# Kernel optimization log

Hardware: AMD Instinct MI355X
Metric: run time of the kernel (lower is better)

The kernel has to match this reference:

```python
import jax, jax.numpy as jnp
import numpy as np

HEADS = 8
NQ = 4  # n_qubits


def _apply_rx(state, q, theta):
    # state: (M,2,2,2,2) complex, theta: (M,)
    c = jnp.cos(theta / 2).astype(jnp.complex64)
    s = (-1j * jnp.sin(theta / 2)).astype(jnp.complex64)
    g = jnp.stack([jnp.stack([c, s], -1), jnp.stack([s, c], -1)], -2)  # (M,2,2)
    st = jnp.moveaxis(state, 1 + q, 1)
    st = jnp.einsum('mab,mb...->ma...', g, st)
    return jnp.moveaxis(st, 1, 1 + q)


def _apply_cnot(state, c, t):
    st = jnp.moveaxis(state, [1 + c, 1 + t], [1, 2])  # (M,2(ctrl),2(tgt),...)
    st = jnp.concatenate([st[:, :1], st[:, 1:, ::-1]], axis=1)
    return jnp.moveaxis(st, [1, 2], [1 + c, 1 + t])


def vqc(x, weights):
    # x: (M,4) embedding angles; weights: (L,4) layer RX angles
    M = x.shape[0]
    state = jnp.zeros((M, 2, 2, 2, 2), jnp.complex64).at[:, 0, 0, 0, 0].set(1.0)
    for q in range(NQ):  # AngleEmbedding (RX)
        state = _apply_rx(state, q, x[:, q])
    for l in range(weights.shape[0]):  # BasicEntanglerLayers
        for q in range(NQ):
            state = _apply_rx(state, q, jnp.broadcast_to(weights[l, q], (M,)))
        for q in range(NQ):
            state = _apply_cnot(state, q, (q + 1) % NQ)
    probs = state.real ** 2 + state.imag ** 2  # (M,2,2,2,2)
    z = [jnp.moveaxis(probs, 1 + q, 1)[:, 0].sum((1, 2, 3))
         - jnp.moveaxis(probs, 1 + q, 1)[:, 1].sum((1, 2, 3)) for q in range(NQ)]
    return jnp.stack(z, -1)  # (M,4) PauliZ expvals


def setup_inputs() -> dict:
    key = jax.random.key(0)
    ks = jax.random.split(key, 24)
    B, S, E = 16, 512, 512
    D = E // HEADS
    f = jax.random.normal
    inp = {
        'query': f(ks[0], (B, S, E), jnp.float32),
        'key': f(ks[1], (B, S, E), jnp.float32),
        'value': f(ks[2], (B, S, E), jnp.float32),
        'mask': jnp.ones((B, S, S), jnp.int32),
        'Wq_in': f(ks[3], (NQ, D), jnp.float32) / np.sqrt(D),
        'bq_in': f(ks[4], (NQ,), jnp.float32) / np.sqrt(D),
        'Wk_in': f(ks[5], (NQ, D), jnp.float32) / np.sqrt(D),
        'bk_in': f(ks[6], (NQ,), jnp.float32) / np.sqrt(D),
        'Wv_in': f(ks[7], (NQ, D), jnp.float32) / np.sqrt(D),
        'bv_in': f(ks[8], (NQ,), jnp.float32) / np.sqrt(D),
        'wvq': f(ks[9], (1, NQ), jnp.float32),
        'wvk': f(ks[10], (1, NQ), jnp.float32),
        'wvv': f(ks[11], (1, NQ), jnp.float32),
        'Wq': f(ks[12], (D, NQ), jnp.float32) / np.sqrt(NQ),
        'bq': f(ks[13], (D,), jnp.float32) / np.sqrt(NQ),
        'Wk': f(ks[14], (D, NQ), jnp.float32) / np.sqrt(NQ),
        'bk': f(ks[15], (D,), jnp.float32) / np.sqrt(NQ),
        'Wv': f(ks[16], (D, NQ), jnp.float32) / np.sqrt(NQ),
        'bv': f(ks[17], (D,), jnp.float32) / np.sqrt(NQ),
        'Wo': f(ks[18], (E, 2 * E), jnp.float32) / np.sqrt(2 * E),
        'bo': f(ks[19], (E,), jnp.float32) / np.sqrt(2 * E),
    }
    return inp


def reference(query, key, value, mask, Wq_in, bq_in, Wk_in, bk_in, Wv_in, bv_in,
              wvq, wvk, wvv, Wq, bq, Wk, bk, Wv, bv, Wo, bo):
    B, S, E = query.shape
    H = HEADS
    D = E // H

    def project(x, W_in, b_in, w_vqc, W_out, b_out):
        xh = x.reshape(B, S, H, D)
        xin = jnp.einsum('bshd,qd->bshq', xh, W_in) + b_in  # (B,S,H,NQ)
        xq = vqc(xin.reshape(-1, NQ), w_vqc).reshape(B, S, H, NQ)
        return jnp.einsum('bshq,dq->bshd', xq, W_out) + b_out  # (B,S,H,D)

    Q = project(query, Wq_in, bq_in, wvq, Wq, bq)
    K = project(key, Wk_in, bk_in, wvk, Wk, bk)
    V = project(value, Wv_in, bv_in, wvv, Wv, bv)

    energy = jnp.einsum('bqhd,bkhd->bhqk', Q, K)
    # NOTE: original masked_fill result is discarded (no-op); scale is depth/2
    # due to Python precedence (depth**1/2 == depth/2). Reproduced faithfully.
    attn = jax.nn.softmax(energy / (D / 2.0), axis=-1)
    out = jnp.einsum('bhqv,bvhd->bqhd', attn, V).reshape(B, S, H * D)
    Qf = Q.reshape(B, S, H * D)
    cat = jnp.concatenate([Qf, out], axis=-1)  # (B,S,2E)
    return cat @ Wo.T + bo
```

## Files before the change

kernel.cpp:

```cpp
#include <hip/hip_runtime.h>
#include <hip/hip_bf16.h>

#define B_ 16
#define S_ 512
#define E_ 512
#define H_ 8
#define D_ 64

typedef __hip_bfloat16 bf16;
typedef unsigned short u16;
typedef __attribute__((ext_vector_type(8))) short short8;
typedef __attribute__((ext_vector_type(4))) float floatx4;

__device__ __forceinline__ u16 f2b(float x) {
    bf16 h = __float2bfloat16(x);
    return *reinterpret_cast<u16*>(&h);
}
__device__ __forceinline__ short8 ld8(const u16* p) { return *(const short8*)p; }

__global__ __launch_bounds__(256) void wconv_kernel(
    const float* __restrict__ Wo, u16* __restrict__ Wb)
{
    const int i = (blockIdx.x * 256 + threadIdx.x) * 8;
    const float4 a = *(const float4*)&Wo[i];
    const float4 b = *(const float4*)&Wo[i + 4];
    u16 tmp[8] __attribute__((aligned(16)));
    tmp[0] = f2b(a.x); tmp[1] = f2b(a.y); tmp[2] = f2b(a.z); tmp[3] = f2b(a.w);
    tmp[4] = f2b(b.x); tmp[5] = f2b(b.y); tmp[6] = f2b(b.z); tmp[7] = f2b(b.w);
    *(short8*)&Wb[i] = *(short8*)tmp;
}

__global__ __launch_bounds__(256) void proj_kernel(
    const float* __restrict__ q_in, const float* __restrict__ k_in, const float* __restrict__ v_in,
    const float* __restrict__ Wq_in, const float* __restrict__ bq_in,
    const float* __restrict__ Wk_in, const float* __restrict__ bk_in,
    const float* __restrict__ Wv_in, const float* __restrict__ bv_in,
    const float* __restrict__ wvq, const float* __restrict__ wvk, const float* __restrict__ wvv,
    const float* __restrict__ Wq, const float* __restrict__ bq,
    const float* __restrict__ Wk, const float* __restrict__ bk,
    const float* __restrict__ Wv, const float* __restrict__ bv,
    u16* __restrict__ Qb, u16* __restrict__ Kb, u16* __restrict__ Vb)
{
    const int wave = threadIdx.x >> 6;
    const int lane = threadIdx.x & 63;
    const int g = blockIdx.x * 4 + wave;
    const int p = g >> 16;
    const int m = g & 0xFFFF;
    const int h = m & 7;
    const int s = (m >> 3) & 511;
    const int b = m >> 12;

    const float *X, *Win, *bin, *wv, *Wout, *bout;
    u16* dst;
    if (p == 0)      { X = q_in; Win = Wq_in; bin = bq_in; wv = wvq; Wout = Wq; bout = bq; dst = Qb; }
    else if (p == 1) { X = k_in; Win = Wk_in; bin = bk_in; wv = wvk; Wout = Wk; bout = bk; dst = Kb; }
    else             { X = v_in; Win = Wv_in; bin = bv_in; wv = wvv; Wout = Wv; bout = bv; dst = Vb; }

    const int q = lane >> 4;
    const int dsub = lane & 15;
    const float* xp = X + ((size_t)(b * S_ + s)) * E_ + h * 64;
    const float* wp = Win + q * 64;

    float part = 0.f;
#pragma unroll
    for (int j = 0; j < 4; ++j)
        part += xp[dsub + 16 * j] * wp[dsub + 16 * j];
#pragma unroll
    for (int off = 8; off >= 1; off >>= 1)
        part += __shfl_xor(part, off, 64);

    const float theta = part + bin[q] + wv[q];
    const float c  = __cosf(theta);
    const float ca = __shfl_xor(c, 16, 64);
    const float cb = __shfl_xor(c, 32, 64);
    const float cd = __shfl_xor(ca, 32, 64);

    const float c0 = (q == 0) ? c : (q == 1) ? ca : (q == 2) ? cb : cd;
    const float c1 = (q == 1) ? c : (q == 0) ? ca : (q == 3) ? cb : cd;
    const float c2 = (q == 2) ? c : (q == 3) ? ca : (q == 0) ? cb : cd;
    const float c3 = (q == 3) ? c : (q == 2) ? ca : (q == 1) ? cb : cd;

    const float z0 = c1 * c2 * c3;
    const float z1 = c0 * c1;
    const float z2 = z1 * c2;
    const float z3 = z2 * c3;

    const float4 wo = *(const float4*)&Wout[lane * 4];
    const float out = z0 * wo.x + z1 * wo.y + z2 * wo.z + z3 * wo.w + bout[lane];
    dst[(((size_t)(b * H_ + h)) * S_ + s) * D_ + lane] = f2b(out);
}

__global__ __launch_bounds__(256) void attn_kernel(
    const u16* __restrict__ Qb, const u16* __restrict__ Kb, const u16* __restrict__ Vb,
    u16* __restrict__ Ob)
{
    __shared__ __align__(16) u16 Ks[64][72];
    __shared__ __align__(16) u16 Vt[64][72];
    __shared__ __align__(16) u16 Ps[4][16][80];

    const int t = threadIdx.x, lane = t & 63, w = t >> 6;
    const int bh = blockIdx.x >> 3;
    const int q0 = (blockIdx.x & 7) * 64;
    const int b = bh >> 3, h = bh & 7;

    const u16* Qp = Qb + (size_t)bh * (S_ * D_) + (size_t)q0 * D_;
    const u16* Kp = Kb + (size_t)bh * (S_ * D_);
    const u16* Vp = Vb + (size_t)bh * (S_ * D_);

    const int nl = lane & 15;
    const int kg = (lane >> 4) * 8;

    const short8 qa0 = ld8(&Qp[(w * 16 + nl) * 64 + kg]);
    const short8 qa1 = ld8(&Qp[(w * 16 + nl) * 64 + kg + 32]);

    floatx4 of[4];
    float l_run[4] = {0.f, 0.f, 0.f, 0.f};
#pragma unroll
    for (int nt = 0; nt < 4; ++nt) of[nt] = 0.f;

    for (int ch = 0; ch < 8; ++ch) {
        __syncthreads();
        for (int i = t; i < 512; i += 256) {
            const int r = i & 63, c = (i >> 6) * 8;
            *(short8*)&Ks[r][c] = ld8(&Kp[(ch * 64 + r) * 64 + c]);
        }
        for (int i = t; i < 512; i += 256) {
            const int r = i & 63, c = (i >> 6) * 8;
            short8 v = ld8(&Vp[(ch * 64 + r) * 64 + c]);
#pragma unroll
            for (int j = 0; j < 8; ++j) Vt[c + j][r] = (u16)((short*)&v)[j];
        }
        __syncthreads();

        floatx4 sf[4];
#pragma unroll
        for (int nt = 0; nt < 4; ++nt) sf[nt] = 0.f;
#pragma unroll
        for (int nt = 0; nt < 4; ++nt) {
            sf[nt] = __builtin_amdgcn_mfma_f32_16x16x32_bf16(qa0, ld8(&Ks[nt * 16 + nl][kg]), sf[nt], 0, 0, 0);
            sf[nt] = __builtin_amdgcn_mfma_f32_16x16x32_bf16(qa1, ld8(&Ks[nt * 16 + nl][kg + 32]), sf[nt], 0, 0, 0);
        }

        const int prow = (lane >> 4) * 4;
#pragma unroll
        for (int nt = 0; nt < 4; ++nt) {
#pragma unroll
            for (int r = 0; r < 4; ++r) {
                const float pv = __expf(sf[nt][r] * 0.03125f);
                l_run[r] += pv;
                Ps[w][prow + r][nt * 16 + nl] = f2b(pv);
            }
        }

        const short8 pa0 = ld8(&Ps[w][nl][kg]);
        const short8 pa1 = ld8(&Ps[w][nl][kg + 32]);
#pragma unroll
        for (int nt = 0; nt < 4; ++nt) {
            of[nt] = __builtin_amdgcn_mfma_f32_16x16x32_bf16(pa0, ld8(&Vt[nt * 16 + nl][kg]), of[nt], 0, 0, 0);
            of[nt] = __builtin_amdgcn_mfma_f32_16x16x32_bf16(pa1, ld8(&Vt[nt * 16 + nl][kg + 32]), of[nt], 0, 0, 0);
        }
    }

    float inv[4];
#pragma unroll
    for (int r = 0; r < 4; ++r) {
        float sum = l_run[r];
#pragma unroll
        for (int off = 1; off < 16; off <<= 1) sum += __shfl_xor(sum, off, 64);
        inv[r] = 1.0f / sum;
    }
    const int srow = q0 + w * 16 + (lane >> 4) * 4;
#pragma unroll
    for (int r = 0; r < 4; ++r) {
        const size_t base = ((size_t)(b * S_ + srow + r)) * E_ + h * 64 + nl;
#pragma unroll
        for (int nt = 0; nt < 4; ++nt)
            Ob[base + nt * 16] = f2b(of[nt][r] * inv[r]);
    }
}

__global__ __launch_bounds__(256) void out_kernel(
    const u16* __restrict__ Qb, const u16* __restrict__ Ob,
    const u16* __restrict__ Wb, const float* __restrict__ bo,
    float* __restrict__ out)
{
    __shared__ __align__(16) u16 As[64][72];
    __shared__ __align__(16) u16 Bs[128][72];

    const int t = threadIdx.x, lane = t & 63, w = t >> 6;
    const int e0 = (blockIdx.x & 3) * 128;
    const int n0 = (blockIdx.x >> 2) * 64;
    const int wr = (w >> 1) * 32, wc = (w & 1) * 64;
    const int nl = lane & 15, kg = (lane >> 4) * 8;

    floatx4 acc[2][4];
#pragma unroll
    for (int i = 0; i < 2; ++i)
#pragma unroll
        for (int j = 0; j < 4; ++j) acc[i][j] = 0.f;

    for (int j0 = 0; j0 < 1024; j0 += 64) {
        for (int i = t; i < 512; i += 256) {
            const int r = i & 63, c = (i >> 6) * 8;
            const int n = n0 + r;
            const u16* src = (j0 < 512)
                ? &Qb[(((size_t)(n >> 9) * 8 + (j0 >> 6)) * 512 + (n & 511)) * 64 + c]
                : &Ob[(size_t)n * 512 + (j0 - 512) + c];
            *(short8*)&As[r][c] = ld8(src);
        }
        for (int i = t; i < 1024; i += 256) {
            const int r = i & 127, c = (i >> 7) * 8;
            *(short8*)&Bs[r][c] = ld8(&Wb[(size_t)(e0 + r) * 1024 + j0 + c]);
        }
        __syncthreads();

        short8 af[2][2], bfr[4][2];
#pragma unroll
        for (int mt = 0; mt < 2; ++mt) {
            af[mt][0] = ld8(&As[wr + mt * 16 + nl][kg]);
            af[mt][1] = ld8(&As[wr + mt * 16 + nl][kg + 32]);
        }
#pragma unroll
        for (int nt = 0; nt < 4; ++nt) {
            bfr[nt][0] = ld8(&Bs[wc + nt * 16 + nl][kg]);
            bfr[nt][1] = ld8(&Bs[wc + nt * 16 + nl][kg + 32]);
        }
#pragma unroll
        for (int mt = 0; mt < 2; ++mt)
#pragma unroll
            for (int nt = 0; nt < 4; ++nt) {
                acc[mt][nt] = __builtin_amdgcn_mfma_f32_16x16x32_bf16(af[mt][0], bfr[nt][0], acc[mt][nt], 0, 0, 0);
                acc[mt][nt] = __builtin_amdgcn_mfma_f32_16x16x32_bf16(af[mt][1], bfr[nt][1], acc[mt][nt], 0, 0, 0);
            }
        __syncthreads();
    }

    const int prow = (lane >> 4) * 4;
#pragma unroll
    for (int mt = 0; mt < 2; ++mt)
#pragma unroll
        for (int r = 0; r < 4; ++r) {
            const int n = n0 + wr + mt * 16 + prow + r;
#pragma unroll
            for (int nt = 0; nt < 4; ++nt) {
                const int e = e0 + wc + nt * 16 + nl;
                out[(size_t)n * 512 + e] = acc[mt][nt][r] + bo[e];
            }
        }
}

extern "C" void kernel_launch(void* const* d_in, const int* in_sizes, int n_in,
                              void* d_out, int out_size, void* d_ws, size_t ws_size,
                              hipStream_t stream)
{
    const float* q_in  = (const float*)d_in[0];
    const float* k_in  = (const float*)d_in[1];
    const float* v_in  = (const float*)d_in[2];
    const float* Wq_in = (const float*)d_in[4];
    const float* bq_in = (const float*)d_in[5];
    const float* Wk_in = (const float*)d_in[6];
    const float* bk_in = (const float*)d_in[7];
    const float* Wv_in = (const float*)d_in[8];
    const float* bv_in = (const float*)d_in[9];
    const float* wvq   = (const float*)d_in[10];
    const float* wvk   = (const float*)d_in[11];
    const float* wvv   = (const float*)d_in[12];
    const float* Wq    = (const float*)d_in[13];
    const float* bq    = (const float*)d_in[14];
    const float* Wk    = (const float*)d_in[15];
    const float* bk    = (const float*)d_in[16];
    const float* Wv    = (const float*)d_in[17];
    const float* bv    = (const float*)d_in[18];
    const float* Wo    = (const float*)d_in[19];
    const float* bo    = (const float*)d_in[20];

    u16* ws = (u16*)d_ws;
    u16* Qb = ws;
    u16* Kb = ws + (size_t)(1 << 22);
    u16* Vb = ws + (size_t)(2 << 22);
    u16* Ob = ws + (size_t)3 * (1 << 22);
    u16* Wb = ws + (size_t)4 * (1 << 22);

    wconv_kernel<<<256, 256, 0, stream>>>(Wo, Wb);
    proj_kernel<<<49152, 256, 0, stream>>>(q_in, k_in, v_in,
        Wq_in, bq_in, Wk_in, bk_in, Wv_in, bv_in,
        wvq, wvk, wvv, Wq, bq, Wk, bk, Wv, bv,
        Qb, Kb, Vb);
    attn_kernel<<<1024, 256, 0, stream>>>(Qb, Kb, Vb, Ob);
    out_kernel<<<512, 256, 0, stream>>>(Qb, Ob, Wb, bo, (float*)d_out);
}
```

Before: 231.3 us.

## Fold weight conversion into projection kernel and vectorize loads and V transpose

Removes the separate Wo-to-bf16 conversion launch by appending 256 extra blocks to the projection kernel, which handle the conversion. The projection now reads input and weights as float4, gathers the four cosines with direct lane broadcasts, and uses fmaf chains. In the attention kernel, V is transposed into shared memory with packed 32-bit writes of two rows at a time, and the P staging buffer padding shrinks from 80 to 72. These changes aim to cut launch overhead, load instruction count and LDS store count, at the risk of different bank conflict behaviour.

```diff
diff --git a/kernel.cpp b/kernel.cpp
--- a/kernel.cpp
+++ b/kernel.cpp
@@ -18,17 +18,7 @@
 }
 __device__ __forceinline__ short8 ld8(const u16* p) { return *(const short8*)p; }
 
-__global__ __launch_bounds__(256) void wconv_kernel(
-    const float* __restrict__ Wo, u16* __restrict__ Wb)
-{
-    const int i = (blockIdx.x * 256 + threadIdx.x) * 8;
-    const float4 a = *(const float4*)&Wo[i];
-    const float4 b = *(const float4*)&Wo[i + 4];
-    u16 tmp[8] __attribute__((aligned(16)));
-    tmp[0] = f2b(a.x); tmp[1] = f2b(a.y); tmp[2] = f2b(a.z); tmp[3] = f2b(a.w);
-    tmp[4] = f2b(b.x); tmp[5] = f2b(b.y); tmp[6] = f2b(b.z); tmp[7] = f2b(b.w);
-    *(short8*)&Wb[i] = *(short8*)tmp;
-}
+#define PROJ_BLOCKS 49152
 
 __global__ __launch_bounds__(256) void proj_kernel(
     const float* __restrict__ q_in, const float* __restrict__ k_in, const float* __restrict__ v_in,
@@ -39,8 +29,20 @@
     const float* __restrict__ Wq, const float* __restrict__ bq,
     const float* __restrict__ Wk, const float* __restrict__ bk,
     const float* __restrict__ Wv, const float* __restrict__ bv,
+    const float* __restrict__ Wo, u16* __restrict__ Wb,
     u16* __restrict__ Qb, u16* __restrict__ Kb, u16* __restrict__ Vb)
 {
+    if (blockIdx.x >= PROJ_BLOCKS) {
+        const int i = ((blockIdx.x - PROJ_BLOCKS) * 256 + threadIdx.x) * 8;
+        const float4 a = *(const float4*)&Wo[i];
+        const float4 b4 = *(const float4*)&Wo[i + 4];
+        u16 tmp[8] __attribute__((aligned(16)));
+        tmp[0] = f2b(a.x); tmp[1] = f2b(a.y); tmp[2] = f2b(a.z); tmp[3] = f2b(a.w);
+        tmp[4] = f2b(b4.x); tmp[5] = f2b(b4.y); tmp[6] = f2b(b4.z); tmp[7] = f2b(b4.w);
+        *(short8*)&Wb[i] = *(short8*)tmp;
+        return;
+    }
+
     const int wave = threadIdx.x >> 6;
     const int lane = threadIdx.x & 63;
     const int g = blockIdx.x * 4 + wave;
@@ -58,35 +60,31 @@
 
     const int q = lane >> 4;
     const int dsub = lane & 15;
-    const float* xp = X + ((size_t)(b * S_ + s)) * E_ + h * 64;
-    const float* wp = Win + q * 64;
-
-    float part = 0.f;
-#pragma unroll
-    for (int j = 0; j < 4; ++j)
-        part += xp[dsub + 16 * j] * wp[dsub + 16 * j];
+
+    const float4 x4 = *(const float4*)(X + ((size_t)(b * S_ + s)) * E_ + h * 64 + dsub * 4);
+    const float4 w4 = *(const float4*)(Win + q * 64 + dsub * 4);
+
+    float part = x4.x * w4.x + x4.y * w4.y + x4.z * w4.z + x4.w * w4.w;
 #pragma unroll
     for (int off = 8; off >= 1; off >>= 1)
         part += __shfl_xor(part, off, 64);
 
     const float theta = part + bin[q] + wv[q];
-    const float c  = __cosf(theta);
-    const float ca = __shfl_xor(c, 16, 64);
-    const float cb = __shfl_xor(c, 32, 64);
-    const float cd = __shfl_xor(ca, 32, 64);
-
-    const float c0 = (q == 0) ? c : (q == 1) ? ca : (q == 2) ? cb : cd;
-    const float c1 = (q == 1) ? c : (q == 0) ? ca : (q == 3) ? cb : cd;
-    const float c2 = (q == 2) ? c : (q == 3) ? ca : (q == 0) ? cb : cd;
-    const float c3 = (q == 3) ? c : (q == 2) ? ca : (q == 1) ? cb : cd;
-
-    const float z0 = c1 * c2 * c3;
+    const float c = __cosf(theta);
+
+    const float c0 = __shfl(c, 0, 64);
+    const float c1 = __shfl(c, 16, 64);
+    const float c2 = __shfl(c, 32, 64);
+    const float c3 = __shfl(c, 48, 64);
+
+    const float tt = c2 * c3;
     const float z1 = c0 * c1;
+    const float z0 = c1 * tt;
     const float z2 = z1 * c2;
-    const float z3 = z2 * c3;
+    const float z3 = z1 * tt;
 
     const float4 wo = *(const float4*)&Wout[lane * 4];
-    const float out = z0 * wo.x + z1 * wo.y + z2 * wo.z + z3 * wo.w + bout[lane];
+    const float out = fmaf(z0, wo.x, fmaf(z1, wo.y, fmaf(z2, wo.z, fmaf(z3, wo.w, bout[lane]))));
     dst[(((size_t)(b * H_ + h)) * S_ + s) * D_ + lane] = f2b(out);
 }
 
@@ -96,7 +94,7 @@
 {
     __shared__ __align__(16) u16 Ks[64][72];
     __shared__ __align__(16) u16 Vt[64][72];
-    __shared__ __align__(16) u16 Ps[4][16][80];
+    __shared__ __align__(16) u16 Ps[4][16][72];
 
     const int t = threadIdx.x, lane = t & 63, w = t >> 6;
     const int bh = blockIdx.x >> 3;
@@ -118,17 +116,23 @@
 #pragma unroll
     for (int nt = 0; nt < 4; ++nt) of[nt] = 0.f;
 
+    const int vr0 = (t & 31) * 2, vc = (t >> 5) * 8;
+
     for (int ch = 0; ch < 8; ++ch) {
         __syncthreads();
         for (int i = t; i < 512; i += 256) {
             const int r = i & 63, c = (i >> 6) * 8;
             *(short8*)&Ks[r][c] = ld8(&Kp[(ch * 64 + r) * 64 + c]);
         }
-        for (int i = t; i < 512; i += 256) {
-            const int r = i & 63, c = (i >> 6) * 8;
-            short8 v = ld8(&Vp[(ch * 64 + r) * 64 + c]);
-#pragma unroll
-            for (int j = 0; j < 8; ++j) Vt[c + j][r] = (u16)((short*)&v)[j];
+        {
+            short8 va = ld8(&Vp[(ch * 64 + vr0) * 64 + vc]);
+            short8 vb = ld8(&Vp[(ch * 64 + vr0 + 1) * 64 + vc]);
+#pragma unroll
+            for (int j = 0; j < 8; ++j) {
+                const unsigned pack = (u16)((short*)&va)[j] |
+                                      ((unsigned)(u16)((short*)&vb)[j] << 16);
+                *(unsigned*)&Vt[vc + j][vr0] = pack;
+            }
         }
         __syncthreads();
 
@@ -281,11 +285,10 @@
     u16* Ob = ws + (size_t)3 * (1 << 22);
     u16* Wb = ws + (size_t)4 * (1 << 22);
 
-    wconv_kernel<<<256, 256, 0, stream>>>(Wo, Wb);
-    proj_kernel<<<49152, 256, 0, stream>>>(q_in, k_in, v_in,
+    proj_kernel<<<PROJ_BLOCKS + 256, 256, 0, stream>>>(q_in, k_in, v_in,
         Wq_in, bq_in, Wk_in, bk_in, Wv_in, bv_in,
         wvq, wvk, wvv, Wq, bq, Wk, bk, Wv, bv,
-        Qb, Kb, Vb);
+        Wo, Wb, Qb, Kb, Vb);
     attn_kernel<<<1024, 256, 0, stream>>>(Qb, Kb, Vb, Ob);
     out_kernel<<<512, 256, 0, stream>>>(Qb, Ob, Wb, bo, (float*)d_out);
 }
```

Result: faster. 225.9 us (-2.3%).
